# Kernel tuning notes

Measured on AMD Instinct MI355X. Metric: run time of the kernel, lower is better.

## Reference

```python
import jax, jax.numpy as jnp
import numpy as np

N_NODES = 50000
N_EDGES = 600000
D_FEAT = 128


def setup_inputs() -> dict:
    key = jax.random.key(0)
    ks = jax.random.split(key, 10)
    x = jax.random.normal(ks[0], (N_NODES, D_FEAT), dtype=jnp.float32)
    src = jax.random.randint(ks[1], (N_EDGES,), 0, N_NODES, dtype=jnp.int32)
    dst = jax.random.randint(ks[2], (N_EDGES,), 0, N_NODES, dtype=jnp.int32)
    w1 = jax.random.normal(ks[3], (1, D_FEAT), dtype=jnp.float32) * 0.05
    Wd1 = jax.random.normal(ks[4], (D_FEAT, 64), dtype=jnp.float32) * 0.05
    b1 = jnp.zeros((64,), dtype=jnp.float32)
    w2 = jax.random.normal(ks[5], (1, 64), dtype=jnp.float32) * 0.05
    Wd2 = jax.random.normal(ks[6], (64, 32), dtype=jnp.float32) * 0.05
    b2 = jnp.zeros((32,), dtype=jnp.float32)
    Wout = jax.random.normal(ks[7], (32, 4), dtype=jnp.float32) * 0.05
    bout = jnp.zeros((4,), dtype=jnp.float32)
    return {"x": x, "src": src, "dst": dst, "w1": w1, "Wd1": Wd1, "b1": b1,
            "w2": w2, "Wd2": Wd2, "b2": b2, "Wout": Wout, "bout": bout}


def _spmm(src, dst, h):
    # A @ h for COO adjacency (edge src -> dst contributes h[src] into row dst)
    return jax.ops.segment_sum(h[src], dst, num_segments=N_NODES)


def reference(x, src, dst, w1, Wd1, b1, w2, Wd2, b2, Wout, bout):
    # input_layer is an Input wrapper: identity. Dropout is identity at inference.
    h = _spmm(src, dst, x) * w1          # GraphLayer 1: SpMM + elementwise scale
    h = h @ Wd1 + b1                     # Dense(64), linear activation
    h = _spmm(src, dst, h) * w2          # GraphLayer 2
    h = h @ Wd2 + b2                     # Dense(32)
    logits = h @ Wout + bout             # Dense(4)
    return jax.nn.softmax(logits, axis=-1)
```

## Files before the change

kernel.cpp:

```cpp
#include <hip/hip_runtime.h>
#include <hip/hip_bf16.h>

#define D_FEAT 128
#define NP 64
#define NP_SHIFT 6
#define P_PARTS 782
#define CAP 1024
#define EPB 2048


__global__ __launch_bounds__(256) void fused_xw_bucket_kernel(
    const float4* __restrict__ x4,
    const int* __restrict__ src,
    const int* __restrict__ dst,
    const float* __restrict__ w1,  const float* __restrict__ Wd1,
    const float* __restrict__ b1,  const float* __restrict__ w2,
    const float* __restrict__ Wd2, const float* __restrict__ b2,
    const float* __restrict__ Wout, const float* __restrict__ bout,
    int* __restrict__ partFill, int* __restrict__ edgeBuf,
    float* __restrict__ gc, float4* __restrict__ u4,
    int nN, int nE, int xwBlocks)
{
    __shared__ int sm[2 * P_PARTS];
    int t = threadIdx.x;

    if ((int)blockIdx.x < xwBlocks) {
        float* T2   = (float*)sm;
        float* Wall = (float*)sm + 256;
        {
            int m = t >> 2, j = t & 3;
            float s = 0.f;
            for (int p = 0; p < 32; ++p) s += Wd2[m * 32 + p] * Wout[p * 4 + j];
            T2[t] = w2[m] * s;
        }
        __syncthreads();
        for (int idx = t; idx < 512; idx += 256) {
            int k = idx >> 2, j = idx & 3;
            float s = 0.f;
            for (int m = 0; m < 64; ++m) s += Wd1[k * 64 + m] * T2[m * 4 + j];
            Wall[idx] = w1[k] * s;
        }
        if (blockIdx.x == 0 && t < 4) {
            float s = 0.f;
            for (int m = 0; m < 64; ++m) s += b1[m] * T2[m * 4 + t];
            gc[t] = s;
            float s2 = 0.f;
            for (int p = 0; p < 32; ++p) s2 += b2[p] * Wout[p * 4 + t];
            gc[4 + t] = s2 + bout[t];
        }
        __syncthreads();
        int r = blockIdx.x * 256 + t;
        if (r < nN) {
            const float4* W = (const float4*)Wall;
            float4 acc = make_float4(0.f, 0.f, 0.f, 0.f);
            #pragma unroll 8
            for (int k4 = 0; k4 < 32; ++k4) {
                float4 xv = x4[(size_t)r * 32 + k4];
                float4 w0 = W[4 * k4 + 0];
                float4 wv1 = W[4 * k4 + 1];
                float4 wv2 = W[4 * k4 + 2];
                float4 wv3 = W[4 * k4 + 3];
                acc.x += xv.x * w0.x + xv.y * wv1.x + xv.z * wv2.x + xv.w * wv3.x;
                acc.y += xv.x * w0.y + xv.y * wv1.y + xv.z * wv2.y + xv.w * wv3.y;
                acc.z += xv.x * w0.z + xv.y * wv1.z + xv.z * wv2.z + xv.w * wv3.z;
                acc.w += xv.x * w0.w + xv.y * wv1.w + xv.z * wv2.w + xv.w * wv3.w;
            }
            u4[r] = acc;
        }
    } else {
        int b = blockIdx.x - xwBlocks;
        int* hist = sm;
        int* base = sm + P_PARTS;
        for (int p = t; p < P_PARTS; p += 256) hist[p] = 0;
        __syncthreads();
        const int4* dst4 = (const int4*)dst;
        const int4* src4 = (const int4*)src;
        int nE4  = nE >> 2;
        int beg4 = b * (EPB / 4) + t;
        int end4 = min(b * (EPB / 4) + (EPB / 4), nE4);
        for (int i = beg4; i < end4; i += 256) {
            int4 d4 = dst4[i];
            atomicAdd(&hist[d4.x >> NP_SHIFT], 1);
            atomicAdd(&hist[d4.y >> NP_SHIFT], 1);
            atomicAdd(&hist[d4.z >> NP_SHIFT], 1);
            atomicAdd(&hist[d4.w >> NP_SHIFT], 1);
        }
        __syncthreads();
        for (int p = t; p < P_PARTS; p += 256) {
            int h = hist[p];
            base[p] = h ? atomicAdd(&partFill[p], h) : 0;
        }
        __syncthreads();
        for (int i = beg4; i < end4; i += 256) {
            int4 d4 = dst4[i];
            int4 s4 = src4[i];
            #pragma unroll
            for (int j = 0; j < 4; ++j) {
                int d = (j == 0) ? d4.x : (j == 1) ? d4.y : (j == 2) ? d4.z : d4.w;
                int s = (j == 0) ? s4.x : (j == 1) ? s4.y : (j == 2) ? s4.z : s4.w;
                int p = d >> NP_SHIFT;
                int rank = atomicSub(&hist[p], 1) - 1;
                int pos = base[p] + rank;
                if (pos < CAP)
                    edgeBuf[p * CAP + pos] = s | ((d & (NP - 1)) << 16);
            }
        }
    }
}

__global__ __launch_bounds__(256) void spmm_part_kernel(
    const int* __restrict__ partFill,
    const int* __restrict__ edgeBuf,
    const float4* __restrict__ in4,
    const float* __restrict__ gc, int gcOff,
    float4* __restrict__ out4, int nN, int doSoftmax)
{
    __shared__ float acc[4 * NP];
    int t = threadIdx.x, p = blockIdx.x;
    acc[t] = 0.f;
    __syncthreads();
    int n = min(partFill[p], CAP);
    const int4* eb4 = (const int4*)(edgeBuf + p * CAP);
    int i0 = t * 4;
    if (i0 < n) {
        int4 e4 = eb4[t];
        int   ne = n - i0;
        float4 v0 = in4[e4.x & 0xFFFF];
        float4 v1 = (ne > 1) ? in4[e4.y & 0xFFFF] : make_float4(0, 0, 0, 0);
        float4 v2 = (ne > 2) ? in4[e4.z & 0xFFFF] : make_float4(0, 0, 0, 0);
        float4 v3 = (ne > 3) ? in4[e4.w & 0xFFFF] : make_float4(0, 0, 0, 0);
        int d0 = e4.x >> 16, d1 = e4.y >> 16, d2 = e4.z >> 16, d3 = e4.w >> 16;
        atomicAdd(&acc[0 * NP + d0], v0.x);
        atomicAdd(&acc[1 * NP + d0], v0.y);
        atomicAdd(&acc[2 * NP + d0], v0.z);
        atomicAdd(&acc[3 * NP + d0], v0.w);
        if (ne > 1) {
            atomicAdd(&acc[0 * NP + d1], v1.x);
            atomicAdd(&acc[1 * NP + d1], v1.y);
            atomicAdd(&acc[2 * NP + d1], v1.z);
            atomicAdd(&acc[3 * NP + d1], v1.w);
        }
        if (ne > 2) {
            atomicAdd(&acc[0 * NP + d2], v2.x);
            atomicAdd(&acc[1 * NP + d2], v2.y);
            atomicAdd(&acc[2 * NP + d2], v2.z);
            atomicAdd(&acc[3 * NP + d2], v2.w);
        }
        if (ne > 3) {
            atomicAdd(&acc[0 * NP + d3], v3.x);
            atomicAdd(&acc[1 * NP + d3], v3.y);
            atomicAdd(&acc[2 * NP + d3], v3.z);
            atomicAdd(&acc[3 * NP + d3], v3.w);
        }
    }
    __syncthreads();
    if (t < NP) {
        int node = p * NP + t;
        if (node < nN) {
            float lx = acc[0 * NP + t] + gc[gcOff + 0];
            float ly = acc[1 * NP + t] + gc[gcOff + 1];
            float lz = acc[2 * NP + t] + gc[gcOff + 2];
            float lw = acc[3 * NP + t] + gc[gcOff + 3];
            if (doSoftmax) {
                float m = fmaxf(fmaxf(lx, ly), fmaxf(lz, lw));
                float ex = __expf(lx - m);
                float ey = __expf(ly - m);
                float ez = __expf(lz - m);
                float ew = __expf(lw - m);
                float r = 1.f / (ex + ey + ez + ew);
                out4[node] = make_float4(ex * r, ey * r, ez * r, ew * r);
            } else {
                out4[node] = make_float4(lx, ly, lz, lw);
            }
        }
    }
}

extern "C" void kernel_launch(void* const* d_in, const int* in_sizes, int n_in,
                              void* d_out, int out_size, void* d_ws, size_t ws_size,
                              hipStream_t stream)
{
    const float* x    = (const float*)d_in[0];
    const int*   src  = (const int*)d_in[1];
    const int*   dst  = (const int*)d_in[2];
    const float* w1   = (const float*)d_in[3];
    const float* Wd1  = (const float*)d_in[4];
    const float* b1   = (const float*)d_in[5];
    const float* w2   = (const float*)d_in[6];
    const float* Wd2  = (const float*)d_in[7];
    const float* b2   = (const float*)d_in[8];
    const float* Wout = (const float*)d_in[9];
    const float* bout = (const float*)d_in[10];

    const int nE = in_sizes[1];
    const int nN = in_sizes[0] / D_FEAT;

    float* ws = (float*)d_ws;
    float* gc = ws;
    float* u  = ws + 16;
    float* v  = u + (size_t)nN * 4;
    int* partFill = (int*)(v + (size_t)nN * 4);
    int* edgeBuf  = partFill + ((P_PARTS + 63) & ~63);

    const int xwBlocks = (nN + 255) / 256;
    const int bkBlocks = (nE + EPB - 1) / EPB;

    hipMemsetAsync(partFill, 0, P_PARTS * sizeof(int), stream);
    fused_xw_bucket_kernel<<<xwBlocks + bkBlocks, 256, 0, stream>>>(
        (const float4*)x, src, dst, w1, Wd1, b1, w2, Wd2, b2, Wout, bout,
        partFill, edgeBuf, gc, (float4*)u, nN, nE, xwBlocks);
    spmm_part_kernel<<<P_PARTS, 256, 0, stream>>>(partFill, edgeBuf,
                                                  (const float4*)u, gc, 0,
                                                  (float4*)v, nN, 0);
    spmm_part_kernel<<<P_PARTS, 256, 0, stream>>>(partFill, edgeBuf,
                                                  (const float4*)v, gc, 4,
                                                  (float4*)d_out, nN, 1);
}
```

Baseline: 146.0 us.

## Merge memset, bucket, and two SpMM passes into one cooperative kernel

Replaces the memset plus three kernel launches with a single cooperative kernel of 512 persistent blocks. Grid-wide syncs separate the phases: zeroing, the projection/bucketing pass, and the two SpMM passes, with each block looping over partitions. The bucketing phase now loads both int4 chunks up front instead of looping. The aim is to remove launch gaps and per-kernel tail effects, at the cost of grid.sync overhead and a fixed grid that must all be co-resident; if the cooperative launch fails it falls back to separate launches.

```diff
diff --git a/kernel.cpp b/kernel.cpp
--- a/kernel.cpp
+++ b/kernel.cpp
@@ -1,5 +1,8 @@
 #include <hip/hip_runtime.h>
 #include <hip/hip_bf16.h>
+#include <hip/hip_cooperative_groups.h>
+
+namespace cg = cooperative_groups;
 
 #define D_FEAT 128
 #define NP 64
@@ -7,116 +10,117 @@
 #define P_PARTS 782
 #define CAP 1024
 #define EPB 2048
-
-
-__global__ __launch_bounds__(256) void fused_xw_bucket_kernel(
-    const float4* __restrict__ x4,
-    const int* __restrict__ src,
-    const int* __restrict__ dst,
-    const float* __restrict__ w1,  const float* __restrict__ Wd1,
-    const float* __restrict__ b1,  const float* __restrict__ w2,
+#define XW_BLOCKS 196
+#define BK_BLOCKS 293
+#define GRID 512
+
+
+__device__ __forceinline__ void phase_xw(
+    int b, int t, int* sm, const float4* __restrict__ x4,
+    const float* __restrict__ w1, const float* __restrict__ Wd1,
+    const float* __restrict__ b1, const float* __restrict__ w2,
     const float* __restrict__ Wd2, const float* __restrict__ b2,
     const float* __restrict__ Wout, const float* __restrict__ bout,
-    int* __restrict__ partFill, int* __restrict__ edgeBuf,
-    float* __restrict__ gc, float4* __restrict__ u4,
-    int nN, int nE, int xwBlocks)
-{
-    __shared__ int sm[2 * P_PARTS];
-    int t = threadIdx.x;
-
-    if ((int)blockIdx.x < xwBlocks) {
-        float* T2   = (float*)sm;
-        float* Wall = (float*)sm + 256;
-        {
-            int m = t >> 2, j = t & 3;
-            float s = 0.f;
-            for (int p = 0; p < 32; ++p) s += Wd2[m * 32 + p] * Wout[p * 4 + j];
-            T2[t] = w2[m] * s;
-        }
-        __syncthreads();
-        for (int idx = t; idx < 512; idx += 256) {
-            int k = idx >> 2, j = idx & 3;
-            float s = 0.f;
-            for (int m = 0; m < 64; ++m) s += Wd1[k * 64 + m] * T2[m * 4 + j];
-            Wall[idx] = w1[k] * s;
-        }
-        if (blockIdx.x == 0 && t < 4) {
-            float s = 0.f;
-            for (int m = 0; m < 64; ++m) s += b1[m] * T2[m * 4 + t];
-            gc[t] = s;
-            float s2 = 0.f;
-            for (int p = 0; p < 32; ++p) s2 += b2[p] * Wout[p * 4 + t];
-            gc[4 + t] = s2 + bout[t];
-        }
-        __syncthreads();
-        int r = blockIdx.x * 256 + t;
-        if (r < nN) {
-            const float4* W = (const float4*)Wall;
-            float4 acc = make_float4(0.f, 0.f, 0.f, 0.f);
-            #pragma unroll 8
-            for (int k4 = 0; k4 < 32; ++k4) {
-                float4 xv = x4[(size_t)r * 32 + k4];
-                float4 w0 = W[4 * k4 + 0];
-                float4 wv1 = W[4 * k4 + 1];
-                float4 wv2 = W[4 * k4 + 2];
-                float4 wv3 = W[4 * k4 + 3];
-                acc.x += xv.x * w0.x + xv.y * wv1.x + xv.z * wv2.x + xv.w * wv3.x;
-                acc.y += xv.x * w0.y + xv.y * wv1.y + xv.z * wv2.y + xv.w * wv3.y;
-                acc.z += xv.x * w0.z + xv.y * wv1.z + xv.z * wv2.z + xv.w * wv3.z;
-                acc.w += xv.x * w0.w + xv.y * wv1.w + xv.z * wv2.w + xv.w * wv3.w;
-            }
-            u4[r] = acc;
-        }
-    } else {
-        int b = blockIdx.x - xwBlocks;
-        int* hist = sm;
-        int* base = sm + P_PARTS;
-        for (int p = t; p < P_PARTS; p += 256) hist[p] = 0;
-        __syncthreads();
-        const int4* dst4 = (const int4*)dst;
-        const int4* src4 = (const int4*)src;
-        int nE4  = nE >> 2;
-        int beg4 = b * (EPB / 4) + t;
-        int end4 = min(b * (EPB / 4) + (EPB / 4), nE4);
-        for (int i = beg4; i < end4; i += 256) {
-            int4 d4 = dst4[i];
-            atomicAdd(&hist[d4.x >> NP_SHIFT], 1);
-            atomicAdd(&hist[d4.y >> NP_SHIFT], 1);
-            atomicAdd(&hist[d4.z >> NP_SHIFT], 1);
-            atomicAdd(&hist[d4.w >> NP_SHIFT], 1);
-        }
-        __syncthreads();
-        for (int p = t; p < P_PARTS; p += 256) {
-            int h = hist[p];
-            base[p] = h ? atomicAdd(&partFill[p], h) : 0;
-        }
-        __syncthreads();
-        for (int i = beg4; i < end4; i += 256) {
-            int4 d4 = dst4[i];
-            int4 s4 = src4[i];
-            #pragma unroll
-            for (int j = 0; j < 4; ++j) {
-                int d = (j == 0) ? d4.x : (j == 1) ? d4.y : (j == 2) ? d4.z : d4.w;
-                int s = (j == 0) ? s4.x : (j == 1) ? s4.y : (j == 2) ? s4.z : s4.w;
-                int p = d >> NP_SHIFT;
-                int rank = atomicSub(&hist[p], 1) - 1;
-                int pos = base[p] + rank;
-                if (pos < CAP)
-                    edgeBuf[p * CAP + pos] = s | ((d & (NP - 1)) << 16);
-            }
-        }
-    }
-}
-
-__global__ __launch_bounds__(256) void spmm_part_kernel(
-    const int* __restrict__ partFill,
-    const int* __restrict__ edgeBuf,
-    const float4* __restrict__ in4,
-    const float* __restrict__ gc, int gcOff,
-    float4* __restrict__ out4, int nN, int doSoftmax)
-{
-    __shared__ float acc[4 * NP];
-    int t = threadIdx.x, p = blockIdx.x;
+    float* __restrict__ gc, float4* __restrict__ u4, int nN)
+{
+    float* T2   = (float*)sm;
+    float* Wall = (float*)sm + 256;
+    {
+        int m = t >> 2, j = t & 3;
+        float s = 0.f;
+        for (int p = 0; p < 32; ++p) s += Wd2[m * 32 + p] * Wout[p * 4 + j];
+        T2[t] = w2[m] * s;
+    }
+    __syncthreads();
+    for (int idx = t; idx < 512; idx += 256) {
+        int k = idx >> 2, j = idx & 3;
+        float s = 0.f;
+        for (int m = 0; m < 64; ++m) s += Wd1[k * 64 + m] * T2[m * 4 + j];
+        Wall[idx] = w1[k] * s;
+    }
+    if (b == 0 && t < 4) {
+        float s = 0.f;
+        for (int m = 0; m < 64; ++m) s += b1[m] * T2[m * 4 + t];
+        gc[t] = s;
+        float s2 = 0.f;
+        for (int p = 0; p < 32; ++p) s2 += b2[p] * Wout[p * 4 + t];
+        gc[4 + t] = s2 + bout[t];
+    }
+    __syncthreads();
+    int r = b * 256 + t;
+    if (r < nN) {
+        const float4* W = (const float4*)Wall;
+        float4 acc = make_float4(0.f, 0.f, 0.f, 0.f);
+        #pragma unroll 8
+        for (int k4 = 0; k4 < 32; ++k4) {
+            float4 xv = x4[(size_t)r * 32 + k4];
+            float4 a0 = W[4 * k4 + 0];
+            float4 a1 = W[4 * k4 + 1];
+            float4 a2 = W[4 * k4 + 2];
+            float4 a3 = W[4 * k4 + 3];
+            acc.x += xv.x * a0.x + xv.y * a1.x + xv.z * a2.x + xv.w * a3.x;
+            acc.y += xv.x * a0.y + xv.y * a1.y + xv.z * a2.y + xv.w * a3.y;
+            acc.z += xv.x * a0.z + xv.y * a1.z + xv.z * a2.z + xv.w * a3.z;
+            acc.w += xv.x * a0.w + xv.y * a1.w + xv.z * a2.w + xv.w * a3.w;
+        }
+        u4[r] = acc;
+    }
+}
+
+__device__ __forceinline__ void phase_bucket(
+    int bb, int t, int* sm,
+    const int* __restrict__ src, const int* __restrict__ dst,
+    int* __restrict__ partFill, int* __restrict__ edgeBuf, int nE)
+{
+    int* hist = sm;
+    int* base = sm + P_PARTS;
+    for (int p = t; p < P_PARTS; p += 256) hist[p] = 0;
+    __syncthreads();
+    const int4* dst4 = (const int4*)dst;
+    const int4* src4 = (const int4*)src;
+    int nE4  = nE >> 2;
+    int b4   = bb * (EPB / 4);
+    int end4 = min(b4 + EPB / 4, nE4);
+    int ia = b4 + t, ib = b4 + 256 + t;
+    bool va = ia < end4, vb = ib < end4;
+    int4 da, sa, db, sb;
+    if (va) { da = dst4[ia]; sa = src4[ia]; }
+    if (vb) { db = dst4[ib]; sb = src4[ib]; }
+    if (va) {
+        atomicAdd(&hist[da.x >> NP_SHIFT], 1);
+        atomicAdd(&hist[da.y >> NP_SHIFT], 1);
+        atomicAdd(&hist[da.z >> NP_SHIFT], 1);
+        atomicAdd(&hist[da.w >> NP_SHIFT], 1);
+    }
+    if (vb) {
+        atomicAdd(&hist[db.x >> NP_SHIFT], 1);
+        atomicAdd(&hist[db.y >> NP_SHIFT], 1);
+        atomicAdd(&hist[db.z >> NP_SHIFT], 1);
+        atomicAdd(&hist[db.w >> NP_SHIFT], 1);
+    }
+    __syncthreads();
+    for (int p = t; p < P_PARTS; p += 256) {
+        int h = hist[p];
+        base[p] = h ? atomicAdd(&partFill[p], h) : 0;
+    }
+    __syncthreads();
+    auto place = [&](int d, int s) {
+        int p = d >> NP_SHIFT;
+        int rank = atomicSub(&hist[p], 1) - 1;
+        int pos = base[p] + rank;
+        if (pos < CAP)
+            edgeBuf[p * CAP + pos] = s | ((d & (NP - 1)) << 16);
+    };
+    if (va) { place(da.x, sa.x); place(da.y, sa.y); place(da.z, sa.z); place(da.w, sa.w); }
+    if (vb) { place(db.x, sb.x); place(db.y, sb.y); place(db.z, sb.z); place(db.w, sb.w); }
+}
+
+__device__ __forceinline__ void spmm_part(
+    int p, int t, float* acc,
+    const int* __restrict__ partFill, const int* __restrict__ edgeBuf,
+    const float4* __restrict__ in4, const float* __restrict__ gc, int gcOff,
+    float4* __restrict__ out4, int nN, bool doSoftmax)
+{
     acc[t] = 0.f;
     __syncthreads();
     int n = min(partFill[p], CAP);
@@ -124,7 +128,7 @@
     int i0 = t * 4;
     if (i0 < n) {
         int4 e4 = eb4[t];
-        int   ne = n - i0;
+        int ne = n - i0;
         float4 v0 = in4[e4.x & 0xFFFF];
         float4 v1 = (ne > 1) ? in4[e4.y & 0xFFFF] : make_float4(0, 0, 0, 0);
         float4 v2 = (ne > 2) ? in4[e4.z & 0xFFFF] : make_float4(0, 0, 0, 0);
@@ -174,45 +178,112 @@
             }
         }
     }
+    __syncthreads();
+}
+
+__global__ __launch_bounds__(256, 4) void mega_kernel(
+    const float4* __restrict__ x4,
+    const int* __restrict__ src, const int* __restrict__ dst,
+    const float* __restrict__ w1, const float* __restrict__ Wd1,
+    const float* __restrict__ b1, const float* __restrict__ w2,
+    const float* __restrict__ Wd2, const float* __restrict__ b2,
+    const float* __restrict__ Wout, const float* __restrict__ bout,
+    int* __restrict__ partFill, int* __restrict__ edgeBuf,
+    float* __restrict__ gc, float4* __restrict__ u4, float4* __restrict__ v4,
+    float4* __restrict__ out4, int nN, int nE)
+{
+    __shared__ int sm[2 * P_PARTS];
+    cg::grid_group grid = cg::this_grid();
+    int t = threadIdx.x, b = blockIdx.x;
+
+    for (int zi = b * 256 + t; zi < P_PARTS; zi += GRID * 256) partFill[zi] = 0;
+    grid.sync();
+
+    if (b < XW_BLOCKS)
+        phase_xw(b, t, sm, x4, w1, Wd1, b1, w2, Wd2, b2, Wout, bout, gc, u4, nN);
+    else if (b < XW_BLOCKS + BK_BLOCKS)
+        phase_bucket(b - XW_BLOCKS, t, sm, src, dst, partFill, edgeBuf, nE);
+    grid.sync();
+
+    for (int p = b; p < P_PARTS; p += GRID)
+        spmm_part(p, t, (float*)sm, partFill, edgeBuf, u4, gc, 0, v4, nN, false);
+    grid.sync();
+
+    for (int p = b; p < P_PARTS; p += GRID)
+        spmm_part(p, t, (float*)sm, partFill, edgeBuf, v4, gc, 4, out4, nN, true);
+}
+
+__global__ __launch_bounds__(256) void xw_bucket_kernel(
+    const float4* __restrict__ x4,
+    const int* __restrict__ src, const int* __restrict__ dst,
+    const float* __restrict__ w1, const float* __restrict__ Wd1,
+    const float* __restrict__ b1, const float* __restrict__ w2,
+    const float* __restrict__ Wd2, const float* __restrict__ b2,
+    const float* __restrict__ Wout, const float* __restrict__ bout,
+    int* __restrict__ partFill, int* __restrict__ edgeBuf,
+    float* __restrict__ gc, float4* __restrict__ u4, int nN, int nE)
+{
+    __shared__ int sm[2 * P_PARTS];
+    int t = threadIdx.x, b = blockIdx.x;
+    if (b < XW_BLOCKS)
+        phase_xw(b, t, sm, x4, w1, Wd1, b1, w2, Wd2, b2, Wout, bout, gc, u4, nN);
+    else
+        phase_bucket(b - XW_BLOCKS, t, sm, src, dst, partFill, edgeBuf, nE);
+}
+
+__global__ __launch_bounds__(256) void spmm_kernel_sa(
+    const int* __restrict__ partFill, const int* __restrict__ edgeBuf,
+    const float4* __restrict__ in4, const float* __restrict__ gc, int gcOff,
+    float4* __restrict__ out4, int nN, int doSoftmax)
+{
+    __shared__ float acc[4 * NP];
+    spmm_part(blockIdx.x, threadIdx.x, acc, partFill, edgeBuf, in4, gc, gcOff,
+              out4, nN, doSoftmax != 0);
 }
 
 extern "C" void kernel_launch(void* const* d_in, const int* in_sizes, int n_in,
                               void* d_out, int out_size, void* d_ws, size_t ws_size,
                               hipStream_t stream)
 {
-    const float* x    = (const float*)d_in[0];
-    const int*   src  = (const int*)d_in[1];
-    const int*   dst  = (const int*)d_in[2];
-    const float* w1   = (const float*)d_in[3];
-    const float* Wd1  = (const float*)d_in[4];
-    const float* b1   = (const float*)d_in[5];
-    const float* w2   = (const float*)d_in[6];
-    const float* Wd2  = (const float*)d_in[7];
-    const float* b2   = (const float*)d_in[8];
-    const float* Wout = (const float*)d_in[9];
-    const float* bout = (const float*)d_in[10];
-
-    const int nE = in_sizes[1];
-    const int nN = in_sizes[0] / D_FEAT;
+    const float4* x4  = (const float4*)d_in[0];
+    const int* srcp   = (const int*)d_in[1];
+    const int* dstp   = (const int*)d_in[2];
+    const float* w1p  = (const float*)d_in[3];
+    const float* Wd1p = (const float*)d_in[4];
+    const float* b1p  = (const float*)d_in[5];
+    const float* w2p  = (const float*)d_in[6];
+    const float* Wd2p = (const float*)d_in[7];
+    const float* b2p  = (const float*)d_in[8];
+    const float* Woutp = (const float*)d_in[9];
+    const float* boutp = (const float*)d_in[10];
+
+    int nE = in_sizes[1];
+    int nN = in_sizes[0] / D_FEAT;
 
     float* ws = (float*)d_ws;
-    float* gc = ws;
-    float* u  = ws + 16;
-    float* v  = u + (size_t)nN * 4;
+    float* gcp = ws;
+    float* u   = ws + 16;
+    float* v   = u + (size_t)nN * 4;
     int* partFill = (int*)(v + (size_t)nN * 4);
-    int* edgeBuf  = partFill + ((P_PARTS + 63) & ~63);
-
-    const int xwBlocks = (nN + 255) / 256;
-    const int bkBlocks = (nE + EPB - 1) / EPB;
-
-    hipMemsetAsync(partFill, 0, P_PARTS * sizeof(int), stream);
-    fused_xw_bucket_kernel<<<xwBlocks + bkBlocks, 256, 0, stream>>>(
-        (const float4*)x, src, dst, w1, Wd1, b1, w2, Wd2, b2, Wout, bout,
-        partFill, edgeBuf, gc, (float4*)u, nN, nE, xwBlocks);
-    spmm_part_kernel<<<P_PARTS, 256, 0, stream>>>(partFill, edgeBuf,
-                                                  (const float4*)u, gc, 0,
-                                                  (float4*)v, nN, 0);
-    spmm_part_kernel<<<P_PARTS, 256, 0, stream>>>(partFill, edgeBuf,
-                                                  (const float4*)v, gc, 4,
-                                                  (float4*)d_out, nN, 1);
-}
+    int* edgeBuf  = partFill + 1024;
+    float4* u4p = (float4*)u;
+    float4* v4p = (float4*)v;
+    float4* o4  = (float4*)d_out;
+
+    void* args[] = { &x4, &srcp, &dstp, &w1p, &Wd1p, &b1p, &w2p, &Wd2p, &b2p,
+                     &Woutp, &boutp, &partFill, &edgeBuf, &gcp, &u4p, &v4p,
+                     &o4, &nN, &nE };
+    hipError_t err = hipLaunchCooperativeKernel((const void*)mega_kernel,
+                                                dim3(GRID), dim3(256),
+                                                args, 0, stream);
+    if (err != hipSuccess) {
+        hipMemsetAsync(partFill, 0, P_PARTS * sizeof(int), stream);
+        xw_bucket_kernel<<<XW_BLOCKS + BK_BLOCKS, 256, 0, stream>>>(
+            x4, srcp, dstp, w1p, Wd1p, b1p, w2p, Wd2p, b2p, Woutp, boutp,
+            partFill, edgeBuf, gcp, u4p, nN, nE);
+        spmm_kernel_sa<<<P_PARTS, 256, 0, stream>>>(partFill, edgeBuf, u4p,
+                                                    gcp, 0, v4p, nN, 0);
+        spmm_kernel_sa<<<P_PARTS, 256, 0, stream>>>(partFill, edgeBuf, v4p,
+                                                    gcp, 4, o4, nN, 1);
+    }
+}
```

After: 316.7 us. 117% more time.
